# Performance work log

Measured on AMD Instinct MI355X. Metric: run time of the kernel, lower is better.

Reference implementation:

```python
import jax, jax.numpy as jnp
import numpy as np

DIM = 512

def setup_inputs() -> dict:
    key = jax.random.key(0)
    k1, k2, k3 = jax.random.split(key, 3)
    x = jax.random.normal(k1, (4, DIM, 64, 64), dtype=jnp.float32)
    w1 = jax.random.normal(k2, (DIM, DIM), dtype=jnp.float32) * (DIM ** -0.5)
    w2 = jax.random.normal(k3, (DIM, DIM), dtype=jnp.float32) * (DIM ** -0.5)
    return {"x": x, "w1": w1, "w2": w2}

def reference(x, w1, w2):
    b, c, h, w = x.shape
    scale = c ** -0.5
    # [b, n, c] with n = h*w spatial tokens
    f = x.reshape(b, c, h * w).transpose(0, 2, 1)
    q = jnp.einsum('bnc,dc->bnd', f, w1)          # linear1 (no bias)
    attn = jnp.einsum('bnd,bmd->bnm', q, f) * scale
    attn = jax.nn.softmax(attn, axis=-1)
    v = jnp.einsum('bnc,dc->bnd', f, w2)          # linear2 (no bias)
    mixed = jnp.einsum('bnm,bmd->bnd', attn, v)
    return mixed.transpose(0, 2, 1).reshape(b, c, h, w)
```

## Files before the change

kernel.cpp:

```cpp
#include <hip/hip_runtime.h>
#include <stdint.h>


typedef __attribute__((ext_vector_type(8)))  short          short8;
typedef __attribute__((ext_vector_type(4)))  float          f32x4;
typedef __attribute__((ext_vector_type(4)))  unsigned short u16x4;
typedef __attribute__((ext_vector_type(8)))  unsigned short u16x8;

#define N_TOK 4096
#define CDIM  512
#define NT    64
#define WSCALE (1.4426950408889634f * 0.04419417382415922f)

static __device__ __forceinline__ unsigned short f2bf(float f){
  unsigned int u = __builtin_bit_cast(unsigned int, f);
  u += 0x7fffu + ((u >> 16) & 1u);
  return (unsigned short)(u >> 16);
}
static __device__ __forceinline__ unsigned int pk2bf(float a, float b){
  unsigned int ua = __builtin_bit_cast(unsigned int, a);
  ua += 0x7fffu + ((ua >> 16) & 1u);
  unsigned int ub = __builtin_bit_cast(unsigned int, b);
  ub += 0x7fffu + ((ub >> 16) & 1u);
  return (ua >> 16) | (ub & 0xffff0000u);
}
static __device__ __forceinline__ void gl_lds16(const void* g, void* l){
  __builtin_amdgcn_global_load_lds((__attribute__((address_space(1))) void*)g,
                                   (__attribute__((address_space(3))) void*)l,
                                   16, 0, 0);
}

__global__ void k_castw(const float* __restrict__ w1, const float* __restrict__ w2,
                        unsigned short* __restrict__ w1b, unsigned short* __restrict__ w2b){
  int i = blockIdx.x * 256 + threadIdx.x;
  float4 a = ((const float4*)w1)[i];
  float4 c = ((const float4*)w2)[i];
  u16x4 oa = { f2bf(a.x*WSCALE), f2bf(a.y*WSCALE), f2bf(a.z*WSCALE), f2bf(a.w*WSCALE) };
  u16x4 oc = { f2bf(c.x), f2bf(c.y), f2bf(c.z), f2bf(c.w) };
  *(u16x4*)(w1b + (size_t)i*4) = oa;
  *(u16x4*)(w2b + (size_t)i*4) = oc;
}

__global__ void k_transpose(const float* __restrict__ x, unsigned short* __restrict__ Kb){
  __shared__ float tile[64][65];
  const int b = blockIdx.z, c0 = blockIdx.y*64, n0 = blockIdx.x*64;
  const int t = threadIdx.x;
#pragma unroll
  for(int i=0;i<4;i++){
    int flat = i*256 + t;
    int row = flat>>4, ch = flat&15;
    float4 v = *(const float4*)(x + ((size_t)(b*CDIM + c0 + row))*N_TOK + n0 + ch*4);
    tile[row][ch*4+0]=v.x; tile[row][ch*4+1]=v.y; tile[row][ch*4+2]=v.z; tile[row][ch*4+3]=v.w;
  }
  __syncthreads();
#pragma unroll
  for(int i=0;i<2;i++){
    int flat = i*256 + t;
    int nr = flat>>3, cc = flat&7;
    u16x8 o;
#pragma unroll
    for(int e=0;e<8;e++) o[e] = f2bf(tile[cc*8+e][nr]);
    *(u16x8*)(Kb + ((size_t)b*N_TOK + n0 + nr)*CDIM + c0 + cc*8) = o;
  }
}

__global__ __launch_bounds__(256, 2)
void k_gemm_bt(const unsigned short* __restrict__ A, const unsigned short* __restrict__ B,
               unsigned short* __restrict__ C,
               long Abstride, long Bbstride, long Cbstride, int ldc)
{
  __shared__ unsigned short Asm[128*32];
  __shared__ unsigned short Bsm[128*32];
  const int b = blockIdx.z;
  const unsigned short* Ab = A + (size_t)b*Abstride;
  const unsigned short* Bb = B + (size_t)b*Bbstride;
  unsigned short* Cb = C + (size_t)b*Cbstride;
  const int t = threadIdx.x, w = t>>6, lane = t&63;
  const int wr = w>>1, wc = w&1;
  const size_t am0 = (size_t)blockIdx.x*128;
  const size_t bn0 = (size_t)blockIdx.y*128;

  f32x4 acc[4][4];
#pragma unroll
  for(int i=0;i<4;i++)
#pragma unroll
    for(int j=0;j<4;j++)
#pragma unroll
      for(int r=0;r<4;r++) acc[i][j][r]=0.f;

  for(int k0=0;k0<CDIM;k0+=32){
#pragma unroll
    for(int i=0;i<2;i++){
      int flat = i*256 + t;
      int row = flat>>2, ch = flat&3;
      gl_lds16(Ab + (am0+row)*CDIM + k0 + ch*8, &Asm[(size_t)(i*256 + w*64)*8]);
    }
#pragma unroll
    for(int i=0;i<2;i++){
      int flat = i*256 + t;
      int row = flat>>2, ch = flat&3;
      gl_lds16(Bb + (bn0+row)*CDIM + k0 + ch*8, &Bsm[(size_t)(i*256 + w*64)*8]);
    }
    __syncthreads();
    short8 af[4], bfr[4];
#pragma unroll
    for(int i=0;i<4;i++){
      af[i]  = *(const short8*)&Asm[(wr*64 + i*16 + (lane&15))*32 + (lane>>4)*8];
      bfr[i] = *(const short8*)&Bsm[(wc*64 + i*16 + (lane&15))*32 + (lane>>4)*8];
    }
#pragma unroll
    for(int i=0;i<4;i++)
#pragma unroll
      for(int j=0;j<4;j++)
        acc[i][j] = __builtin_amdgcn_mfma_f32_16x16x32_bf16(af[i], bfr[j], acc[i][j], 0,0,0);
    __syncthreads();
  }
#pragma unroll
  for(int i=0;i<4;i++)
#pragma unroll
    for(int j=0;j<4;j++){
      size_t m0 = am0 + wr*64 + i*16 + (lane>>4)*4;
      size_t n  = bn0 + wc*64 + j*16 + (lane&15);
#pragma unroll
      for(int r=0;r<4;r++)
        Cb[(m0+r)*(size_t)ldc + n] = f2bf(acc[i][j][r]);
    }
}

__global__ __launch_bounds__(512, 1)
void k_attn(const unsigned short* __restrict__ Qb, const unsigned short* __restrict__ Kb,
            const unsigned short* __restrict__ Vt,
            float* __restrict__ Op0, float* __restrict__ Op1,
            float* __restrict__ Lp)
{
  __shared__ unsigned short Ks[2][32*512];
  __shared__ unsigned short Vs[2][512*32];
  const int nb = blockIdx.x, b = blockIdx.y, kvh = blockIdx.z;
  const int t = threadIdx.x, w = t>>6, lane = t&63;
  const int g = lane>>4, q15 = lane&15;
  const int qrow = nb*128 + w*16 + q15;
  const size_t bK = (size_t)b*N_TOK*CDIM;
  const size_t bV = (size_t)b*CDIM*N_TOK;
  const int kvbase = kvh*2048;

  short8 qreg[16];
  {
    const unsigned short* qp = Qb + bK + (size_t)qrow*CDIM + g*8;
#pragma unroll
    for(int cs=0;cs<16;cs++) qreg[cs] = *(const short8*)(qp + cs*32);
  }

  f32x4 accO[32];
#pragma unroll
  for(int dt=0;dt<32;dt++)
#pragma unroll
    for(int r=0;r<4;r++) accO[dt][r]=0.f;

  float lsum = 0.f;

  auto stage = [&](int kt, int bb){
    const int kv0 = kvbase + kt*32;
#pragma unroll
    for(int j=0;j<4;j++){
      int r = w*4 + j;
      gl_lds16(Kb + bK + (size_t)(kv0+r)*CDIM + ((lane ^ (r&7))*8),
               &Ks[bb][(size_t)r*512]);
    }
#pragma unroll
    for(int j=0;j<4;j++){
      int base = (w*4+j)*64;
      int flat = base + lane;
      int d = flat>>2, c4 = flat&3;
      gl_lds16(Vt + bV + (size_t)d*N_TOK + kv0 + ((c4 ^ ((d>>1)&3))*8),
               &Vs[bb][(size_t)base*8]);
    }
  };

  stage(0, 0);
  __syncthreads();

  for(int kt=0; kt<NT; ++kt){
    const int cur = kt&1;
    if(kt<NT-1) stage(kt+1, cur^1);

    const unsigned short* ksb = &Ks[cur][0];
    f32x4 s0, s1;
#pragma unroll
    for(int r=0;r<4;r++){ s0[r]=0.f; s1[r]=0.f; }
    __builtin_amdgcn_s_setprio(1);
#pragma unroll
    for(int cs=0;cs<16;cs++){
      int slot = (cs*4 + g) ^ (q15&7);
      short8 a0 = *(const short8*)(ksb + (size_t)q15*512      + slot*8);
      short8 a1 = *(const short8*)(ksb + (size_t)(16+q15)*512 + slot*8);
      s0 = __builtin_amdgcn_mfma_f32_16x16x32_bf16(a0, qreg[cs], s0, 0,0,0);
      s1 = __builtin_amdgcn_mfma_f32_16x16x32_bf16(a1, qreg[cs], s1, 0,0,0);
    }
    __builtin_amdgcn_s_setprio(0);

    float z[8];
#pragma unroll
    for(int r=0;r<4;r++){ z[r] = exp2f(s0[r]); z[4+r] = exp2f(s1[r]); }
    float ps = z[0]+z[1]+z[2]+z[3]+z[4]+z[5]+z[6]+z[7];
    ps += __shfl_xor(ps, 16);
    ps += __shfl_xor(ps, 32);
    lsum += ps;

    {
      int w0 = (int)pk2bf(z[0], z[1]);
      int w1 = (int)pk2bf(z[2], z[3]);
      int w2 = (int)pk2bf(z[4], z[5]);
      int w3 = (int)pk2bf(z[6], z[7]);
      int srcA = (q15 + ((g&1)<<5)) << 2;
      int srcB = srcA + (16<<2);
      int A00 = __builtin_amdgcn_ds_bpermute(srcA, w0);
      int A01 = __builtin_amdgcn_ds_bpermute(srcA, w1);
      int A10 = __builtin_amdgcn_ds_bpermute(srcA, w2);
      int A11 = __builtin_amdgcn_ds_bpermute(srcA, w3);
      int B00 = __builtin_amdgcn_ds_bpermute(srcB, w0);
      int B01 = __builtin_amdgcn_ds_bpermute(srcB, w1);
      int B10 = __builtin_amdgcn_ds_bpermute(srcB, w2);
      int B11 = __builtin_amdgcn_ds_bpermute(srcB, w3);
      const bool tt = (g>>1) != 0;
      union { int u[4]; short8 v; } pu;
      pu.u[0] = tt ? A10 : A00;
      pu.u[1] = tt ? A11 : A01;
      pu.u[2] = tt ? B10 : B00;
      pu.u[3] = tt ? B11 : B01;
      short8 pf = pu.v;

      const unsigned short* vsb = &Vs[cur][0];
      __builtin_amdgcn_s_setprio(1);
#pragma unroll
      for(int dt=0;dt<32;dt++){
        int vrow = dt*16 + q15;
        int slot = g ^ ((vrow>>1)&3);
        short8 vf = *(const short8*)(vsb + (size_t)vrow*32 + slot*8);
        accO[dt] = __builtin_amdgcn_mfma_f32_16x16x32_bf16(vf, pf, accO[dt], 0,0,0);
      }
      __builtin_amdgcn_s_setprio(0);
    }
    __syncthreads();
  }

  float* Op = kvh ? Op1 : Op0;
#pragma unroll
  for(int dt=0;dt<32;dt++)
#pragma unroll
    for(int r=0;r<4;r++){
      int d = dt*16 + 4*g + r;
      Op[bV + (size_t)d*N_TOK + qrow] = accO[dt][r];
    }
  if(g==0){
    int idx = kvh*16384 + b*4096 + qrow;
    Lp[idx] = lsum;
  }
}

__global__ void k_merge(const float* __restrict__ O1, const float* __restrict__ Lp,
                        float* __restrict__ out)
{
  size_t i4 = ((size_t)blockIdx.x*256 + threadIdx.x) * 4;
  int n = (int)(i4 & 4095);
  int b = (int)(i4 >> 21);
  float4 o0 = *(const float4*)(out + i4);
  float4 o1 = *(const float4*)(O1 + i4);
  float4 l0 = *(const float4*)(Lp + b*4096 + n);
  float4 l1 = *(const float4*)(Lp + 16384 + b*4096 + n);
  float4 r;
#pragma unroll
  for(int e=0;e<4;e++){
    float num = ((const float*)&o0)[e] + ((const float*)&o1)[e];
    float den = ((const float*)&l0)[e] + ((const float*)&l1)[e];
    ((float*)&r)[e] = num / den;
  }
  *(float4*)(out + i4) = r;
}

extern "C" void kernel_launch(void* const* d_in, const int* in_sizes, int n_in,
                              void* d_out, int out_size, void* d_ws, size_t ws_size,
                              hipStream_t stream)
{
  const float* x  = (const float*)d_in[0];
  const float* w1 = (const float*)d_in[1];
  const float* w2 = (const float*)d_in[2];
  float* out = (float*)d_out;

  unsigned short* ws  = (unsigned short*)d_ws;
  unsigned short* w1b = ws;
  unsigned short* w2b = ws + 262144;
  unsigned short* Kb  = ws + 524288;
  unsigned short* Qb  = Kb + (size_t)4*N_TOK*CDIM;
  unsigned short* Vtb = Qb + (size_t)4*N_TOK*CDIM;
  float* O1f = (float*)(Vtb + (size_t)4*N_TOK*CDIM);
  float* Lpf = O1f + (size_t)4*CDIM*N_TOK;

  k_castw    <<<256, 256, 0, stream>>>(w1, w2, w1b, w2b);
  k_transpose<<<dim3(64,8,4), 256, 0, stream>>>(x, Kb);
  k_gemm_bt  <<<dim3(32,4,4), 256, 0, stream>>>(Kb, w1b, Qb,
              (long)N_TOK*CDIM, 0L, (long)N_TOK*CDIM, CDIM);
  k_gemm_bt  <<<dim3(4,32,4), 256, 0, stream>>>(w2b, Kb, Vtb,
              0L, (long)N_TOK*CDIM, (long)CDIM*N_TOK, N_TOK);
  k_attn     <<<dim3(32,4,2), 512, 0, stream>>>(Qb, Kb, Vtb, out, O1f, Lpf);
  k_merge    <<<8192, 256, 0, stream>>>(O1f, Lpf, out);
}
```

Baseline: 285.6 us.

## Software-pipeline QK^T of next tile with PV of current tile in attention

Restructures the attention main loop so the QK^T MFMAs for tile kt+1 are issued before the PV MFMAs for tile kt, with K staged two tiles ahead and V one tile ahead. The exp/bf16 pack/bpermute softmax step then runs after PV, so its latency can overlap with matrix work instead of serialising between the two MFMA phases. The cost is extra live registers for the next-tile scores and the P fragment, plus more complex buffer indexing, which could raise register pressure at 512 threads per block.

After: 284.3 us. No clear change (-0.5%).

```diff
diff --git a/kernel.cpp b/kernel.cpp
--- a/kernel.cpp
+++ b/kernel.cpp
@@ -133,8 +133,10 @@
             float* __restrict__ Op0, float* __restrict__ Op1,
             float* __restrict__ Lp)
 {
-  __shared__ unsigned short Ks[2][32*512];
-  __shared__ unsigned short Vs[2][512*32];
+  __shared__ unsigned short KsA[32*512];
+  __shared__ unsigned short KsB[32*512];
+  __shared__ unsigned short VsA[512*32];
+  __shared__ unsigned short VsB[512*32];
   const int nb = blockIdx.x, b = blockIdx.y, kvh = blockIdx.z;
   const int t = threadIdx.x, w = t>>6, lane = t&63;
   const int g = lane>>4, q15 = lane&15;
@@ -158,33 +160,27 @@
 
   float lsum = 0.f;
 
-  auto stage = [&](int kt, int bb){
+  auto stageK = [&](int kt, unsigned short* dst){
     const int kv0 = kvbase + kt*32;
 #pragma unroll
     for(int j=0;j<4;j++){
       int r = w*4 + j;
       gl_lds16(Kb + bK + (size_t)(kv0+r)*CDIM + ((lane ^ (r&7))*8),
-               &Ks[bb][(size_t)r*512]);
-    }
+               dst + (size_t)r*512);
+    }
+  };
+  auto stageV = [&](int kt, unsigned short* dst){
+    const int kv0 = kvbase + kt*32;
 #pragma unroll
     for(int j=0;j<4;j++){
       int base = (w*4+j)*64;
       int flat = base + lane;
       int d = flat>>2, c4 = flat&3;
       gl_lds16(Vt + bV + (size_t)d*N_TOK + kv0 + ((c4 ^ ((d>>1)&3))*8),
-               &Vs[bb][(size_t)base*8]);
+               dst + (size_t)base*8);
     }
   };
-
-  stage(0, 0);
-  __syncthreads();
-
-  for(int kt=0; kt<NT; ++kt){
-    const int cur = kt&1;
-    if(kt<NT-1) stage(kt+1, cur^1);
-
-    const unsigned short* ksb = &Ks[cur][0];
-    f32x4 s0, s1;
+  auto computeS = [&](const unsigned short* ksb, f32x4& s0, f32x4& s1){
 #pragma unroll
     for(int r=0;r<4;r++){ s0[r]=0.f; s1[r]=0.f; }
     __builtin_amdgcn_s_setprio(1);
@@ -197,7 +193,8 @@
       s1 = __builtin_amdgcn_mfma_f32_16x16x32_bf16(a1, qreg[cs], s1, 0,0,0);
     }
     __builtin_amdgcn_s_setprio(0);
-
+  };
+  auto computeSM = [&](const f32x4& s0, const f32x4& s1) -> short8 {
     float z[8];
 #pragma unroll
     for(int r=0;r<4;r++){ z[r] = exp2f(s0[r]); z[4+r] = exp2f(s1[r]); }
@@ -205,41 +202,64 @@
     ps += __shfl_xor(ps, 16);
     ps += __shfl_xor(ps, 32);
     lsum += ps;
-
-    {
-      int w0 = (int)pk2bf(z[0], z[1]);
-      int w1 = (int)pk2bf(z[2], z[3]);
-      int w2 = (int)pk2bf(z[4], z[5]);
-      int w3 = (int)pk2bf(z[6], z[7]);
-      int srcA = (q15 + ((g&1)<<5)) << 2;
-      int srcB = srcA + (16<<2);
-      int A00 = __builtin_amdgcn_ds_bpermute(srcA, w0);
-      int A01 = __builtin_amdgcn_ds_bpermute(srcA, w1);
-      int A10 = __builtin_amdgcn_ds_bpermute(srcA, w2);
-      int A11 = __builtin_amdgcn_ds_bpermute(srcA, w3);
-      int B00 = __builtin_amdgcn_ds_bpermute(srcB, w0);
-      int B01 = __builtin_amdgcn_ds_bpermute(srcB, w1);
-      int B10 = __builtin_amdgcn_ds_bpermute(srcB, w2);
-      int B11 = __builtin_amdgcn_ds_bpermute(srcB, w3);
-      const bool tt = (g>>1) != 0;
-      union { int u[4]; short8 v; } pu;
-      pu.u[0] = tt ? A10 : A00;
-      pu.u[1] = tt ? A11 : A01;
-      pu.u[2] = tt ? B10 : B00;
-      pu.u[3] = tt ? B11 : B01;
-      short8 pf = pu.v;
-
-      const unsigned short* vsb = &Vs[cur][0];
-      __builtin_amdgcn_s_setprio(1);
-#pragma unroll
-      for(int dt=0;dt<32;dt++){
-        int vrow = dt*16 + q15;
-        int slot = g ^ ((vrow>>1)&3);
-        short8 vf = *(const short8*)(vsb + (size_t)vrow*32 + slot*8);
-        accO[dt] = __builtin_amdgcn_mfma_f32_16x16x32_bf16(vf, pf, accO[dt], 0,0,0);
-      }
-      __builtin_amdgcn_s_setprio(0);
-    }
+    int w0 = (int)pk2bf(z[0], z[1]);
+    int w1 = (int)pk2bf(z[2], z[3]);
+    int w2 = (int)pk2bf(z[4], z[5]);
+    int w3 = (int)pk2bf(z[6], z[7]);
+    int srcA = (q15 + ((g&1)<<5)) << 2;
+    int srcB = srcA + (16<<2);
+    int A00 = __builtin_amdgcn_ds_bpermute(srcA, w0);
+    int A01 = __builtin_amdgcn_ds_bpermute(srcA, w1);
+    int A10 = __builtin_amdgcn_ds_bpermute(srcA, w2);
+    int A11 = __builtin_amdgcn_ds_bpermute(srcA, w3);
+    int B00 = __builtin_amdgcn_ds_bpermute(srcB, w0);
+    int B01 = __builtin_amdgcn_ds_bpermute(srcB, w1);
+    int B10 = __builtin_amdgcn_ds_bpermute(srcB, w2);
+    int B11 = __builtin_amdgcn_ds_bpermute(srcB, w3);
+    const bool tt = (g>>1) != 0;
+    union { int u[4]; short8 v; } pu;
+    pu.u[0] = tt ? A10 : A00;
+    pu.u[1] = tt ? A11 : A01;
+    pu.u[2] = tt ? B10 : B00;
+    pu.u[3] = tt ? B11 : B01;
+    return pu.v;
+  };
+
+  stageK(0, KsA); stageV(0, VsA); stageK(1, KsB);
+  __syncthreads();
+  short8 pf;
+  {
+    f32x4 s0, s1;
+    computeS(KsA, s0, s1);
+    pf = computeSM(s0, s1);
+  }
+  __syncthreads();
+
+  for(int kt=0; kt<NT; ++kt){
+    const bool odd = (kt&1) != 0;
+    unsigned short* KW = odd ? KsB : KsA;
+    const unsigned short* KR = odd ? KsA : KsB;
+    unsigned short* VW = odd ? VsA : VsB;
+    const unsigned short* VR = odd ? VsB : VsA;
+
+    if(kt+2<NT) stageK(kt+2, KW);
+    if(kt+1<NT) stageV(kt+1, VW);
+
+    f32x4 s0n, s1n;
+    if(kt+1<NT) computeS(KR, s0n, s1n);
+
+    __builtin_amdgcn_s_setprio(1);
+#pragma unroll
+    for(int dt=0;dt<32;dt++){
+      int vrow = dt*16 + q15;
+      int slot = g ^ ((vrow>>1)&3);
+      short8 vf = *(const short8*)(VR + (size_t)vrow*32 + slot*8);
+      accO[dt] = __builtin_amdgcn_mfma_f32_16x16x32_bf16(vf, pf, accO[dt], 0,0,0);
+    }
+    __builtin_amdgcn_s_setprio(0);
+
+    if(kt+1<NT) pf = computeSM(s0n, s1n);
+
     __syncthreads();
   }
 
```

## Share P fragments between paired waves to halve V LDS reads in PV

Applied to the files above, without the earlier changes.

Each pair of waves now exchanges its bf16 P fragment through a small LDS buffer. Each wave then computes the PV product for two query tiles over half of the output channels, so every V fragment read from LDS feeds two MFMAs instead of one. This targets the LDS read bandwidth of the PV stage. The cost is an extra __syncthreads per KV tile plus a small LDS exchange buffer, and the output stores are rearranged to match.

Measured after the change: 274.9 us. 1.04x faster.

```diff
diff --git a/kernel.cpp b/kernel.cpp
--- a/kernel.cpp
+++ b/kernel.cpp
@@ -6,6 +6,7 @@
 typedef __attribute__((ext_vector_type(4)))  float          f32x4;
 typedef __attribute__((ext_vector_type(4)))  unsigned short u16x4;
 typedef __attribute__((ext_vector_type(8)))  unsigned short u16x8;
+typedef __attribute__((ext_vector_type(4)))  unsigned int   u32x4;
 
 #define N_TOK 4096
 #define CDIM  512
@@ -135,9 +136,11 @@
 {
   __shared__ unsigned short Ks[2][32*512];
   __shared__ unsigned short Vs[2][512*32];
+  __shared__ unsigned int   Pex[8][64][4];
   const int nb = blockIdx.x, b = blockIdx.y, kvh = blockIdx.z;
   const int t = threadIdx.x, w = t>>6, lane = t&63;
   const int g = lane>>4, q15 = lane&15;
+  const int dh = w&1;
   const int qrow = nb*128 + w*16 + q15;
   const size_t bK = (size_t)b*N_TOK*CDIM;
   const size_t bV = (size_t)b*CDIM*N_TOK;
@@ -150,11 +153,13 @@
     for(int cs=0;cs<16;cs++) qreg[cs] = *(const short8*)(qp + cs*32);
   }
 
-  f32x4 accO[32];
-#pragma unroll
-  for(int dt=0;dt<32;dt++)
-#pragma unroll
-    for(int r=0;r<4;r++) accO[dt][r]=0.f;
+  f32x4 accO[2][16];
+#pragma unroll
+  for(int s=0;s<2;s++)
+#pragma unroll
+    for(int dt=0;dt<16;dt++)
+#pragma unroll
+      for(int r=0;r<4;r++) accO[s][dt][r]=0.f;
 
   float lsum = 0.f;
 
@@ -206,6 +211,7 @@
     ps += __shfl_xor(ps, 32);
     lsum += ps;
 
+    short8 pf;
     {
       int w0 = (int)pk2bf(z[0], z[1]);
       int w1 = (int)pk2bf(z[2], z[3]);
@@ -227,30 +233,44 @@
       pu.u[1] = tt ? A11 : A01;
       pu.u[2] = tt ? B10 : B00;
       pu.u[3] = tt ? B11 : B01;
-      short8 pf = pu.v;
-
-      const unsigned short* vsb = &Vs[cur][0];
-      __builtin_amdgcn_s_setprio(1);
-#pragma unroll
-      for(int dt=0;dt<32;dt++){
-        int vrow = dt*16 + q15;
-        int slot = g ^ ((vrow>>1)&3);
-        short8 vf = *(const short8*)(vsb + (size_t)vrow*32 + slot*8);
-        accO[dt] = __builtin_amdgcn_mfma_f32_16x16x32_bf16(vf, pf, accO[dt], 0,0,0);
+      pf = pu.v;
+      *(u32x4*)&Pex[w][lane][0] = *(u32x4*)&pu.u[0];
+    }
+    __syncthreads();
+
+    short8 pfP;
+    {
+      u32x4 tmp = *(const u32x4*)&Pex[w^1][lane][0];
+      union { u32x4 u; short8 v; } cc; cc.u = tmp;
+      pfP = cc.v;
+    }
+    const unsigned short* vsb = &Vs[cur][0];
+    __builtin_amdgcn_s_setprio(1);
+#pragma unroll
+    for(int dt=0;dt<16;dt++){
+      int vrow = dh*256 + dt*16 + q15;
+      int slot = g ^ ((vrow>>1)&3);
+      short8 vf = *(const short8*)(vsb + (size_t)vrow*32 + slot*8);
+      accO[0][dt] = __builtin_amdgcn_mfma_f32_16x16x32_bf16(vf, pf,  accO[0][dt], 0,0,0);
+      accO[1][dt] = __builtin_amdgcn_mfma_f32_16x16x32_bf16(vf, pfP, accO[1][dt], 0,0,0);
+    }
+    __builtin_amdgcn_s_setprio(0);
+    __syncthreads();
+  }
+
+  float* Op = kvh ? Op1 : Op0;
+#pragma unroll
+  for(int side=0;side<2;side++){
+    int qw = side ? (w^1) : w;
+    int qr2 = nb*128 + qw*16 + q15;
+#pragma unroll
+    for(int dt=0;dt<16;dt++)
+#pragma unroll
+      for(int r=0;r<4;r++){
+        int d = dh*256 + dt*16 + 4*g + r;
+        Op[bV + (size_t)d*N_TOK + qr2] = accO[side][dt][r];
       }
-      __builtin_amdgcn_s_setprio(0);
-    }
-    __syncthreads();
-  }
-
-  float* Op = kvh ? Op1 : Op0;
-#pragma unroll
-  for(int dt=0;dt<32;dt++)
-#pragma unroll
-    for(int r=0;r<4;r++){
-      int d = dt*16 + 4*g + r;
-      Op[bV + (size_t)d*N_TOK + qrow] = accO[dt][r];
-    }
+  }
   if(g==0){
     int idx = kvh*16384 + b*4096 + qrow;
     Lp[idx] = lsum;
```
